# Performance work log

Measured on AMD Instinct MI355X. Metric: run time of the kernel, lower is better.

The kernel has to match this reference:

```python
import math
import jax, jax.numpy as jnp
import numpy as np

B, S, D, H = 2, 2048, 1024, 16


def setup_inputs() -> dict:
    key = jax.random.key(0)
    ks = jax.random.split(key, 8)
    scale = 1.0 / math.sqrt(D)
    kv_mask = jax.random.randint(ks[1], (B, S), 0, 2).astype(bool)
    kv_mask = kv_mask.at[:, 0].set(True)  # ensure at least one valid kv per batch
    return {
        "q": jax.random.normal(ks[0], (B, S, D), dtype=jnp.float32),
        "kv_mask": kv_mask,
        "Wq": jax.random.normal(ks[2], (D, D), dtype=jnp.float32) * scale,
        "Wk": jax.random.normal(ks[3], (D, D), dtype=jnp.float32) * scale,
        "Wv": jax.random.normal(ks[4], (D, D), dtype=jnp.float32) * scale,
        "Wo": jax.random.normal(ks[5], (D, D), dtype=jnp.float32) * scale,
        "bo": jax.random.normal(ks[6], (D,), dtype=jnp.float32) * 0.01,
        "num_heads": H,
    }


def _pass_with_mask(x, W, mask, b=None):
    # Linear applied everywhere, output zeroed where mask is False (pass_with_mask)
    y = x @ W.T
    if b is not None:
        y = y + b
    return jnp.where(mask[..., None], y, 0.0)


def reference(q, kv_mask, Wq, Wk, Wv, Wo, bo, num_heads):
    b, s, d = q.shape
    hd = d // num_heads
    q_mask = jnp.ones((b, s), dtype=bool)  # default q_mask in the module
    # self-attention: k = v = q
    qh = _pass_with_mask(q, Wq, q_mask).reshape(b, s, num_heads, hd)
    kh = _pass_with_mask(q, Wk, kv_mask).reshape(b, s, num_heads, hd)
    vh = _pass_with_mask(q, Wv, kv_mask).reshape(b, s, num_heads, hd)
    # scores: note the module scales by sqrt(model_dim), NOT sqrt(head_dim)
    scores = jnp.einsum("bqhd,bkhd->bhqk", qh, kh) / math.sqrt(d)
    mask = (q_mask[:, :, None] & kv_mask[:, None, :])[:, None, :, :]  # [b,1,q,k]
    scores = jnp.where(mask, scores, -jnp.inf)
    attn = jax.nn.softmax(scores, axis=-1)
    attn = jnp.where(mask, attn, 0.0)
    out = jnp.einsum("bhqk,bkhd->bqhd", attn, vh).reshape(b, s, d)
    return _pass_with_mask(out, Wo, q_mask, bo)
```

## Files before the change

kernel.cpp:

```cpp
#include <hip/hip_runtime.h>
#include <math.h>

#define B_ 2
#define S_ 2048
#define DM 1024
#define NH 16
#define HD 64

typedef unsigned short u16;
typedef unsigned int u32;
typedef __attribute__((ext_vector_type(8))) short bf16x8;
typedef __attribute__((ext_vector_type(4))) float f32x4;

#define C2SCALE 0.0450842200277800f

__device__ __forceinline__ u16 f2bf(float x) {
  unsigned u = __float_as_uint(x);
  u = (u + 0x7FFFu + ((u >> 16) & 1u)) >> 16;
  return (u16)u;
}

__device__ __forceinline__ u32 cvtpk(float lo, float hi) {
  u32 r;
  asm("v_cvt_pk_bf16_f32 %0, %1, %2" : "=v"(r) : "v"(lo), "v"(hi));
  return r;
}

__device__ __forceinline__ float exp2a(float x) {
  float r;
  asm("v_exp_f32 %0, %1" : "=v"(r) : "v"(x));
  return r;
}

__device__ __forceinline__ void gload_lds16(const u16* g, u16* l) {
  __builtin_amdgcn_global_load_lds((const __attribute__((address_space(1))) void*)g,
                                   (__attribute__((address_space(3))) void*)l, 16, 0, 0);
}

__device__ __forceinline__ int sigpos(int w6) {
  return ((w6 >> 5) << 5) | (((w6 >> 2) & 3) << 3) | (((w6 >> 4) & 1) << 2) | (w6 & 3);
}

__global__ void mask_scan(const int* __restrict__ kvm, int* __restrict__ posb,
                          int* __restrict__ nvb, u16* __restrict__ mwg) {
  const int b = blockIdx.x;
  const int tid = threadIdx.x;
  const int lane = tid & 63, wv = tid >> 6;
  __shared__ int wsum[4];
  int v[8], s = 0;
  const int base = b * S_ + tid * 8;
#pragma unroll
  for (int j = 0; j < 8; j++) { v[j] = kvm[base + j] ? 1 : 0; s += v[j]; }
  int sc = s;
#pragma unroll
  for (int off = 1; off < 64; off <<= 1) {
    int t = __shfl_up(sc, off, 64);
    if (lane >= off) sc += t;
  }
  if (lane == 63) wsum[wv] = sc;
  __syncthreads();
  int woff = 0;
#pragma unroll
  for (int w = 0; w < 4; w++) woff += (w < wv) ? wsum[w] : 0;
  int run = woff + sc - s;
#pragma unroll
  for (int j = 0; j < 8; j++) { posb[base + j] = run; run += v[j]; }
  const int total = wsum[0] + wsum[1] + wsum[2] + wsum[3];
  if (tid == 0) nvb[b] = total;
  for (int i = tid; i < S_; i += 256)
    mwg[b * S_ + (i & ~63) + sigpos(i & 63)] = (i < total) ? 0xFFFFu : 0u;
}

__global__ void cvt_all(const float* __restrict__ q, const float* __restrict__ Wq,
                        const float* __restrict__ Wk, const float* __restrict__ Wv,
                        const float* __restrict__ Wo, const int* __restrict__ nvb,
                        u16* __restrict__ Xbf, u16* __restrict__ Wcat,
                        u16* __restrict__ Wobf, u16* __restrict__ vtbuf) {
  const int NQ4 = (B_ * S_ * DM) / 4;
  const int NW4 = (DM * DM) / 4;
  const int total = NQ4 + 4 * NW4;
  int i = blockIdx.x * blockDim.x + threadIdx.x;
  int stride = gridDim.x * blockDim.x;
  for (int idx = i; idx < B_ * NH * HD * 64; idx += stride) {
    int col = idx & 63;
    int dd = (idx >> 6) & 63;
    int bh = idx >> 12;
    int nv = nvb[bh >> 4];
    int padw = ((nv + 63) & ~63) - nv;
    if (col < padw)
      vtbuf[((size_t)bh * HD + dd) * S_ + nv + col] = 0;
  }
  for (; i < total; i += stride) {
    const float* src;
    u16* dst;
    if (i < NQ4) {
      src = q + (size_t)i * 4; dst = Xbf + (size_t)i * 4;
    } else {
      int t = i - NQ4;
      if (t < NW4)            { src = Wq + (size_t)t * 4; dst = Wcat + (size_t)t * 4; }
      else if (t < 2 * NW4)   { src = Wk + (size_t)(t - NW4) * 4;     dst = Wcat + DM * DM + (size_t)(t - NW4) * 4; }
      else if (t < 3 * NW4)   { src = Wv + (size_t)(t - 2 * NW4) * 4; dst = Wcat + 2 * DM * DM + (size_t)(t - 2 * NW4) * 4; }
      else                    { src = Wo + (size_t)(t - 3 * NW4) * 4; dst = Wobf + (size_t)(t - 3 * NW4) * 4; }
    }
    float4 v = *(const float4*)src;
    ushort4 o;
    o.x = f2bf(v.x); o.y = f2bf(v.y); o.z = f2bf(v.z); o.w = f2bf(v.w);
    *(ushort4*)dst = o;
  }
}

__global__ __launch_bounds__(512, 6) void gemm_bt(
    const u16* __restrict__ A, const u16* __restrict__ Bw,
    u16* __restrict__ qo, u16* __restrict__ ko, u16* __restrict__ vo,
    const int* __restrict__ kvm, const int* __restrict__ posb) {
  __shared__ __align__(16) u16 As[2][64 * 64];
  __shared__ __align__(16) u16 Bs[2][64 * 64];
  const int K = DM;
  const int tid = threadIdx.x;
  const int wv = tid >> 6, lane = tid & 63;
  const int g = lane >> 4, c = lane & 15;
  const int wr = wv >> 1, wc = wv & 1;
  const int L = blockIdx.y * gridDim.x + blockIdx.x;
  const int cpx = (gridDim.x * gridDim.y) >> 3;
  const int Ls = (L & 7) * cpx + (L >> 3);
  const int Mb = (Ls & 31) << 7, Nb = (Ls >> 5) << 7;

  f32x4 acc[2][4];
#pragma unroll
  for (int i = 0; i < 2; i++)
#pragma unroll
    for (int j = 0; j < 4; j++) acc[i][j] = f32x4{0.f, 0.f, 0.f, 0.f};

  const int srow = tid >> 3;
  const int scol8 = tid & 7;
  const int m1 = srow * 2 + (scol8 >> 2);
  const int kkc = (scol8 & 3) * 8;
  const u16* ag = A + (size_t)(Mb + m1) * K + kkc;
  const u16* bg = Bw + (size_t)(Nb + m1) * K + kkc;
  const int slot = scol8 ^ (srow & 7);
  u16* al = &As[0][srow * 64 + slot * 8];
  u16* bl = &Bs[0][srow * 64 + slot * 8];

  bf16x8 ar = *(const bf16x8*)ag;
  bf16x8 br = *(const bf16x8*)bg;
  *(bf16x8*)al = ar;
  *(bf16x8*)bl = br;
  ar = *(const bf16x8*)(ag + 32);
  br = *(const bf16x8*)(bg + 32);
  __syncthreads();

  const int off = ((((c & 1) << 2) | g) ^ (c >> 1)) << 3;
  const int arb = (wr * 16 + (c >> 1)) * 64 + off;
  const int brb = (wc * 32 + (c >> 1)) * 64 + off;

  for (int t = 0; t < 32; ++t) {
    const int cur = t & 1;
    if (t + 1 < 32) {
      const int nb = (cur ^ 1) * 4096;
      *(bf16x8*)(al + nb) = ar;
      *(bf16x8*)(bl + nb) = br;
      if (t + 2 < 32) {
        ar = *(const bf16x8*)(ag + (t + 2) * 32);
        br = *(const bf16x8*)(bg + (t + 2) * 32);
      }
    }
    const u16* AB = &As[cur][0];
    const u16* BB = &Bs[cur][0];
    bf16x8 af[2], bfr[4];
#pragma unroll
    for (int mi = 0; mi < 2; mi++)
      af[mi] = *(const bf16x8*)&AB[arb + mi * 512];
#pragma unroll
    for (int ni = 0; ni < 4; ni++)
      bfr[ni] = *(const bf16x8*)&BB[brb + ni * 512];
#pragma unroll
    for (int mi = 0; mi < 2; mi++)
#pragma unroll
      for (int ni = 0; ni < 4; ni++)
        acc[mi][ni] = __builtin_amdgcn_mfma_f32_16x16x32_bf16(af[mi], bfr[ni], acc[mi][ni], 0, 0, 0);
    asm volatile("s_waitcnt lgkmcnt(0)\n\ts_barrier" ::: "memory");
  }

  const int nbase = Nb + wc * 64 + c;
  const int which = nbase >> 10;
  if (which == 0) {
#pragma unroll
    for (int mi = 0; mi < 2; mi++) {
#pragma unroll
      for (int ni = 0; ni < 4; ni++) {
        int nn = nbase + ni * 16;
        int h = nn >> 6, d = nn & 63;
#pragma unroll
        for (int r = 0; r < 4; r++) {
          int row = Mb + wr * 32 + mi * 16 + g * 4 + r;
          int b0 = row >> 11, s0 = row & 2047;
          qo[(((size_t)(b0 * NH + h)) * S_ + s0) * HD + d] =
              f2bf(acc[mi][ni][r] * C2SCALE);
        }
      }
    }
  } else if (which == 1) {
#pragma unroll
    for (int mi = 0; mi < 2; mi++) {
#pragma unroll
      for (int r = 0; r < 4; r++) {
        int row = Mb + wr * 32 + mi * 16 + g * 4 + r;
        int b0 = row >> 11, s0 = row & 2047;
        if (kvm[b0 * S_ + s0]) {
          int p = posb[b0 * S_ + s0];
#pragma unroll
          for (int ni = 0; ni < 4; ni++) {
            int nn = (nbase + ni * 16) & 1023;
            ko[((size_t)(b0 * NH + (nn >> 6)) * S_ + p) * HD + (nn & 63)] =
                f2bf(acc[mi][ni][r]);
          }
        }
      }
    }
  } else {
#pragma unroll
    for (int mi = 0; mi < 2; mi++) {
#pragma unroll
      for (int r = 0; r < 4; r++) {
        int row = Mb + wr * 32 + mi * 16 + g * 4 + r;
        int b0 = row >> 11, s0 = row & 2047;
        if (kvm[b0 * S_ + s0]) {
          int p = posb[b0 * S_ + s0];
          int dst = (p & ~63) + sigpos(p & 63);
#pragma unroll
          for (int ni = 0; ni < 4; ni++) {
            int nn = (nbase + ni * 16) & 1023;
            vo[((size_t)((b0 * NH + (nn >> 6)) * HD + (nn & 63))) * S_ + dst] =
                f2bf(acc[mi][ni][r]);
          }
        }
      }
    }
  }
}

__global__ __launch_bounds__(256, 4) void gemm_n64(
    const u16* __restrict__ A, const u16* __restrict__ Bw,
    const float* __restrict__ bias, float* __restrict__ fo) {
  __shared__ __align__(16) u16 As[128 * 32];
  __shared__ __align__(16) u16 Bs[64 * 32];
  const int K = DM, N = DM;
  const int tid = threadIdx.x;
  const int wv = tid >> 6, lane = tid & 63;
  const int g = lane >> 4, c = lane & 15;
  const int wr = wv >> 1, wc = wv & 1;
  const int L = blockIdx.x;
  const int Ls = (L & 7) * 64 + (L >> 3);
  const int Mb = (Ls & 31) << 7, Nb = (Ls >> 5) << 6;

  f32x4 acc[4][2];
#pragma unroll
  for (int i = 0; i < 4; i++)
#pragma unroll
    for (int j = 0; j < 2; j++) acc[i][j] = f32x4{0.f, 0.f, 0.f, 0.f};

  for (int kb = 0; kb < K; kb += 32) {
#pragma unroll
    for (int it = 0; it < 2; ++it) {
      int id = it * 256 + tid;
      int m = id >> 2, kk = (id & 3) * 8;
      gload_lds16(A + (size_t)(Mb + m) * K + kb + kk, As + (it * 4 + wv) * 512);
    }
    {
      int m = tid >> 2, kk = (tid & 3) * 8;
      gload_lds16(Bw + (size_t)(Nb + m) * K + kb + kk, Bs + wv * 512);
    }
    __syncthreads();
    bf16x8 af[4], bfr[2];
#pragma unroll
    for (int mi = 0; mi < 4; mi++)
      af[mi] = *(const bf16x8*)(As + (wr * 64 + mi * 16 + c) * 32 + g * 8);
#pragma unroll
    for (int ni = 0; ni < 2; ni++)
      bfr[ni] = *(const bf16x8*)(Bs + (wc * 32 + ni * 16 + c) * 32 + g * 8);
#pragma unroll
    for (int mi = 0; mi < 4; mi++)
#pragma unroll
      for (int ni = 0; ni < 2; ni++)
        acc[mi][ni] = __builtin_amdgcn_mfma_f32_16x16x32_bf16(af[mi], bfr[ni], acc[mi][ni], 0, 0, 0);
    __syncthreads();
  }

#pragma unroll
  for (int mi = 0; mi < 4; mi++) {
#pragma unroll
    for (int ni = 0; ni < 2; ni++) {
      int n = Nb + wc * 32 + ni * 16 + c;
      float bv = bias[n];
#pragma unroll
      for (int r = 0; r < 4; r++) {
        int row = Mb + wr * 64 + mi * 16 + g * 4 + r;
        fo[(size_t)row * N + n] = acc[mi][ni][r] + bv;
      }
    }
  }
}

__global__ __launch_bounds__(512, 4) void attn_kernel(
    const u16* __restrict__ qb, const u16* __restrict__ kb,
    const u16* __restrict__ vtb, const u16* __restrict__ mwg,
    const int* __restrict__ nvb, u16* __restrict__ ob) {
  __shared__ __align__(16) u16 Kl[2][64 * 64];
  __shared__ __align__(16) u16 Vl[2][64 * 64];
  __shared__ __align__(16) u16 MW[S_];

  const int tid = threadIdx.x;
  const int wv = tid >> 6, lane = tid & 63;
  const int g = lane >> 4, c = lane & 15;

  const int L = blockIdx.x;
  const int j = L >> 3;
  const int bh = ((L & 7) << 2) | (j >> 4);
  const int qi = j & 15;
  const int b = bh >> 4, h = bh & 15;
  const int q0 = qi * 128;
  const size_t bhbase = (size_t)bh * (S_ * HD);
  const int NT = (nvb[b] + 63) >> 6;

  ((uint2*)MW)[tid] = ((const uint2*)(mwg + b * S_))[tid];

  bf16x8 qf[2];
#pragma unroll
  for (int ks = 0; ks < 2; ks++)
    qf[ks] = *(const bf16x8*)(qb + bhbase + (size_t)(q0 + wv * 16 + c) * HD + ks * 32 + g * 8);

  f32x4 Oa[4];
#pragma unroll
  for (int di = 0; di < 4; di++) Oa[di] = f32x4{0.f, 0.f, 0.f, 0.f};
  f32x4 lacc = f32x4{0.f, 0.f, 0.f, 0.f};

  union { u32 u[4]; bf16x8 v; } ones;
#pragma unroll
  for (int w = 0; w < 4; w++) ones.u[w] = 0x3F803F80u;

  const int srow = tid >> 3;
  const int scol8 = tid & 7;
  const u16* kg = kb + bhbase + (size_t)srow * HD + scol8 * 8;
  const u16* vg = vtb + bhbase + (size_t)srow * S_ + scol8 * 8;
  const int wslot = scol8 ^ (srow & 7);
  u16* kld = &Kl[0][srow * 64 + wslot * 8];
  u16* vld = &Vl[0][srow * 64 + wslot * 8];

  bf16x8 krg = *(const bf16x8*)kg;
  bf16x8 vrg = *(const bf16x8*)vg;
  *(bf16x8*)kld = krg;
  *(bf16x8*)vld = vrg;
  krg = *(const bf16x8*)(kg + 64 * HD);
  vrg = *(const bf16x8*)(vg + 64);
  __syncthreads();

  const int swz = c & 7;

  for (int t = 0; t < NT; ++t) {
    const int cur = t & 1;
    if (t + 1 < NT) {
      *(bf16x8*)(kld + (cur ^ 1) * 4096) = krg;
      *(bf16x8*)(vld + (cur ^ 1) * 4096) = vrg;
      if (t + 2 < NT) {
        krg = *(const bf16x8*)(kg + (t + 2) * (64 * HD));
        vrg = *(const bf16x8*)(vg + (t + 2) * 64);
      }
    }
    const u16* KB = &Kl[cur][0];
    const u16* VB = &Vl[cur][0];

    f32x4 Sa[4];
#pragma unroll
    for (int ni = 0; ni < 4; ni++) Sa[ni] = f32x4{0.f, 0.f, 0.f, 0.f};
    __builtin_amdgcn_s_setprio(1);
#pragma unroll
    for (int ks = 0; ks < 2; ks++) {
      bf16x8 kf[4];
#pragma unroll
      for (int ni = 0; ni < 4; ni++)
        kf[ni] = *(const bf16x8*)&KB[(ni * 16 + c) * 64 + (((4 * ks + g) ^ swz) * 8)];
#pragma unroll
      for (int ni = 0; ni < 4; ni++)
        Sa[ni] = __builtin_amdgcn_mfma_f32_16x16x32_bf16(kf[ni], qf[ks], Sa[ni], 0, 0, 0);
    }
    __builtin_amdgcn_s_setprio(0);

    bf16x8 Pa[2];
#pragma unroll
    for (int ks = 0; ks < 2; ks++) {
      uint4 mw = *(const uint4*)&MW[t * 64 + ks * 32 + g * 8];
      union { u32 u[4]; bf16x8 v; } pw;
      pw.u[0] = cvtpk(exp2a(Sa[2 * ks][0]), exp2a(Sa[2 * ks][1])) & mw.x;
      pw.u[1] = cvtpk(exp2a(Sa[2 * ks][2]), exp2a(Sa[2 * ks][3])) & mw.y;
      pw.u[2] = cvtpk(exp2a(Sa[2 * ks + 1][0]), exp2a(Sa[2 * ks + 1][1])) & mw.z;
      pw.u[3] = cvtpk(exp2a(Sa[2 * ks + 1][2]), exp2a(Sa[2 * ks + 1][3])) & mw.w;
      Pa[ks] = pw.v;
    }

    __builtin_amdgcn_s_setprio(1);
    lacc = __builtin_amdgcn_mfma_f32_16x16x32_bf16(ones.v, Pa[0], lacc, 0, 0, 0);
    lacc = __builtin_amdgcn_mfma_f32_16x16x32_bf16(ones.v, Pa[1], lacc, 0, 0, 0);
#pragma unroll
    for (int ks = 0; ks < 2; ks++) {
      bf16x8 vf[4];
#pragma unroll
      for (int di = 0; di < 4; di++)
        vf[di] = *(const bf16x8*)&VB[(di * 16 + c) * 64 + (((4 * ks + g) ^ swz) * 8)];
#pragma unroll
      for (int di = 0; di < 4; di++)
        Oa[di] = __builtin_amdgcn_mfma_f32_16x16x32_bf16(vf[di], Pa[ks], Oa[di], 0, 0, 0);
    }
    __builtin_amdgcn_s_setprio(0);

    asm volatile("s_waitcnt lgkmcnt(0)\n\ts_barrier" ::: "memory");
  }

  float inv = 1.f / lacc[0];
  int q = q0 + wv * 16 + c;
  size_t base = ((size_t)(b * S_ + q)) * DM + (size_t)h * HD;
#pragma unroll
  for (int di = 0; di < 4; di++) {
    uint2 o;
    o.x = cvtpk(Oa[di][0] * inv, Oa[di][1] * inv);
    o.y = cvtpk(Oa[di][2] * inv, Oa[di][3] * inv);
    *(uint2*)(ob + base + di * 16 + g * 4) = o;
  }
}

extern "C" void kernel_launch(void* const* d_in, const int* in_sizes, int n_in,
                              void* d_out, int out_size, void* d_ws, size_t ws_size,
                              hipStream_t stream) {
  const float* q  = (const float*)d_in[0];
  const int* kvm  = (const int*)d_in[1];
  const float* Wq = (const float*)d_in[2];
  const float* Wk = (const float*)d_in[3];
  const float* Wv = (const float*)d_in[4];
  const float* Wo = (const float*)d_in[5];
  const float* bo = (const float*)d_in[6];
  float* out = (float*)d_out;
  char* ws = (char*)d_ws;

  u16* Xbf   = (u16*)(ws);
  u16* Wcat  = (u16*)(ws + (8u << 20));
  u16* Wobf  = (u16*)(ws + (14u << 20));
  u16* qbuf  = (u16*)(ws + (16u << 20));
  u16* kbuf  = (u16*)(ws + (24u << 20));
  u16* vtbuf = (u16*)(ws + (32u << 20));
  u16* mwg   = (u16*)(ws + (40u << 20));
  int* posb  = (int*)(ws + (41u << 20));
  int* nvb   = (int*)(ws + (42u << 20));
  u16* obuf  = Xbf;

  mask_scan<<<B_, 256, 0, stream>>>(kvm, posb, nvb, mwg);
  cvt_all<<<2048, 256, 0, stream>>>(q, Wq, Wk, Wv, Wo, nvb, Xbf, Wcat, Wobf, vtbuf);
  gemm_bt<<<dim3(32, 24), 512, 0, stream>>>(Xbf, Wcat, qbuf, kbuf, vtbuf,
                                            kvm, posb);
  attn_kernel<<<512, 512, 0, stream>>>(qbuf, kbuf, vtbuf, mwg, nvb, obuf);
  gemm_n64<<<512, 256, 0, stream>>>(obuf, Wobf, bo, out);
}
```

Baseline: 109.3 us.

## Compact valid KV rows before K/V projection and skip masked-row GEMM tiles

The conversion kernel now also scatters valid (kv_mask true) rows of the bf16 input into a compacted buffer, which reuses the output allocation as scratch. The QKV GEMM is restructured into a 1D grid: Q tiles use the full input, while K/V tiles read the compacted rows and exit early for tiles beyond the valid count. Because roughly half the keys are masked, this cuts about half the K/V projection FLOPs and replaces per-row mask/position lookups in the epilogue with a simple bound check. In exchange it adds an extra scattered write of the input and relies on the output buffer being free until the final GEMM.

```diff
diff --git a/kernel.cpp b/kernel.cpp
--- a/kernel.cpp
+++ b/kernel.cpp
@@ -73,9 +73,11 @@
 
 __global__ void cvt_all(const float* __restrict__ q, const float* __restrict__ Wq,
                         const float* __restrict__ Wk, const float* __restrict__ Wv,
-                        const float* __restrict__ Wo, const int* __restrict__ nvb,
+                        const float* __restrict__ Wo, const int* __restrict__ kvm,
+                        const int* __restrict__ posb, const int* __restrict__ nvb,
                         u16* __restrict__ Xbf, u16* __restrict__ Wcat,
-                        u16* __restrict__ Wobf, u16* __restrict__ vtbuf) {
+                        u16* __restrict__ Wobf, u16* __restrict__ vtbuf,
+                        u16* __restrict__ Xc) {
   const int NQ4 = (B_ * S_ * DM) / 4;
   const int NW4 = (DM * DM) / 4;
   const int total = NQ4 + 4 * NW4;
@@ -91,39 +93,64 @@
       vtbuf[((size_t)bh * HD + dd) * S_ + nv + col] = 0;
   }
   for (; i < total; i += stride) {
-    const float* src;
-    u16* dst;
     if (i < NQ4) {
-      src = q + (size_t)i * 4; dst = Xbf + (size_t)i * 4;
+      float4 v = ((const float4*)q)[i];
+      ushort4 o;
+      o.x = f2bf(v.x); o.y = f2bf(v.y); o.z = f2bf(v.z); o.w = f2bf(v.w);
+      ((ushort4*)Xbf)[i] = o;
+      int row = i >> 8, chunk = i & 255;
+      int b = row >> 11, s = row & 2047;
+      if (kvm[b * S_ + s]) {
+        int p = posb[b * S_ + s];
+        *(ushort4*)(Xc + ((size_t)(b * S_ + p)) * DM + chunk * 4) = o;
+      }
     } else {
       int t = i - NQ4;
+      const float* src;
+      u16* dst;
       if (t < NW4)            { src = Wq + (size_t)t * 4; dst = Wcat + (size_t)t * 4; }
       else if (t < 2 * NW4)   { src = Wk + (size_t)(t - NW4) * 4;     dst = Wcat + DM * DM + (size_t)(t - NW4) * 4; }
       else if (t < 3 * NW4)   { src = Wv + (size_t)(t - 2 * NW4) * 4; dst = Wcat + 2 * DM * DM + (size_t)(t - 2 * NW4) * 4; }
       else                    { src = Wo + (size_t)(t - 3 * NW4) * 4; dst = Wobf + (size_t)(t - 3 * NW4) * 4; }
-    }
-    float4 v = *(const float4*)src;
-    ushort4 o;
-    o.x = f2bf(v.x); o.y = f2bf(v.y); o.z = f2bf(v.z); o.w = f2bf(v.w);
-    *(ushort4*)dst = o;
-  }
-}
-
-__global__ __launch_bounds__(512, 6) void gemm_bt(
-    const u16* __restrict__ A, const u16* __restrict__ Bw,
-    u16* __restrict__ qo, u16* __restrict__ ko, u16* __restrict__ vo,
-    const int* __restrict__ kvm, const int* __restrict__ posb) {
+      float4 v = *(const float4*)src;
+      ushort4 o;
+      o.x = f2bf(v.x); o.y = f2bf(v.y); o.z = f2bf(v.z); o.w = f2bf(v.w);
+      *(ushort4*)dst = o;
+    }
+  }
+}
+
+__global__ __launch_bounds__(512, 6) void gemm_qkv(
+    const u16* __restrict__ Xbf, const u16* __restrict__ Xc,
+    const u16* __restrict__ Wcat, u16* __restrict__ qo, u16* __restrict__ ko,
+    u16* __restrict__ vo, const int* __restrict__ nvb) {
+  const int K = DM;
+  const int Lraw = blockIdx.x;
+  const int Ls = (Lraw & 7) * 96 + (Lraw >> 3);
+
+  int Mb, nglob, bkv = 0, nv = 1 << 30;
+  const u16* Ap;
+  if (Ls < 256) {
+    Mb = (Ls & 31) << 7;
+    nglob = (Ls >> 5) << 7;
+    Ap = Xbf;
+  } else {
+    int L2 = Ls - 256;
+    bkv = L2 >> 8;
+    int L3 = L2 & 255;
+    Mb = (L3 & 15) << 7;
+    nglob = 1024 + ((L3 >> 4) << 7);
+    nv = nvb[bkv];
+    if (Mb >= nv) return;
+    Ap = Xc + (size_t)bkv * S_ * DM;
+  }
+
   __shared__ __align__(16) u16 As[2][64 * 64];
   __shared__ __align__(16) u16 Bs[2][64 * 64];
-  const int K = DM;
   const int tid = threadIdx.x;
   const int wv = tid >> 6, lane = tid & 63;
   const int g = lane >> 4, c = lane & 15;
   const int wr = wv >> 1, wc = wv & 1;
-  const int L = blockIdx.y * gridDim.x + blockIdx.x;
-  const int cpx = (gridDim.x * gridDim.y) >> 3;
-  const int Ls = (L & 7) * cpx + (L >> 3);
-  const int Mb = (Ls & 31) << 7, Nb = (Ls >> 5) << 7;
 
   f32x4 acc[2][4];
 #pragma unroll
@@ -135,8 +162,8 @@
   const int scol8 = tid & 7;
   const int m1 = srow * 2 + (scol8 >> 2);
   const int kkc = (scol8 & 3) * 8;
-  const u16* ag = A + (size_t)(Mb + m1) * K + kkc;
-  const u16* bg = Bw + (size_t)(Nb + m1) * K + kkc;
+  const u16* ag = Ap + (size_t)(Mb + m1) * K + kkc;
+  const u16* bg = Wcat + (size_t)(nglob + m1) * K + kkc;
   const int slot = scol8 ^ (srow & 7);
   u16* al = &As[0][srow * 64 + slot * 8];
   u16* bl = &Bs[0][srow * 64 + slot * 8];
@@ -181,7 +208,7 @@
     asm volatile("s_waitcnt lgkmcnt(0)\n\ts_barrier" ::: "memory");
   }
 
-  const int nbase = Nb + wc * 64 + c;
+  const int nbase = nglob + wc * 64 + c;
   const int which = nbase >> 10;
   if (which == 0) {
 #pragma unroll
@@ -204,14 +231,12 @@
     for (int mi = 0; mi < 2; mi++) {
 #pragma unroll
       for (int r = 0; r < 4; r++) {
-        int row = Mb + wr * 32 + mi * 16 + g * 4 + r;
-        int b0 = row >> 11, s0 = row & 2047;
-        if (kvm[b0 * S_ + s0]) {
-          int p = posb[b0 * S_ + s0];
+        int p = Mb + wr * 32 + mi * 16 + g * 4 + r;
+        if (p < nv) {
 #pragma unroll
           for (int ni = 0; ni < 4; ni++) {
             int nn = (nbase + ni * 16) & 1023;
-            ko[((size_t)(b0 * NH + (nn >> 6)) * S_ + p) * HD + (nn & 63)] =
+            ko[((size_t)(bkv * NH + (nn >> 6)) * S_ + p) * HD + (nn & 63)] =
                 f2bf(acc[mi][ni][r]);
           }
         }
@@ -222,15 +247,13 @@
     for (int mi = 0; mi < 2; mi++) {
 #pragma unroll
       for (int r = 0; r < 4; r++) {
-        int row = Mb + wr * 32 + mi * 16 + g * 4 + r;
-        int b0 = row >> 11, s0 = row & 2047;
-        if (kvm[b0 * S_ + s0]) {
-          int p = posb[b0 * S_ + s0];
+        int p = Mb + wr * 32 + mi * 16 + g * 4 + r;
+        if (p < nv) {
           int dst = (p & ~63) + sigpos(p & 63);
 #pragma unroll
           for (int ni = 0; ni < 4; ni++) {
             int nn = (nbase + ni * 16) & 1023;
-            vo[((size_t)((b0 * NH + (nn >> 6)) * HD + (nn & 63))) * S_ + dst] =
+            vo[((size_t)((bkv * NH + (nn >> 6)) * HD + (nn & 63))) * S_ + dst] =
                 f2bf(acc[mi][ni][r]);
           }
         }
@@ -449,12 +472,13 @@
   u16* mwg   = (u16*)(ws + (40u << 20));
   int* posb  = (int*)(ws + (41u << 20));
   int* nvb   = (int*)(ws + (42u << 20));
+  u16* Xc    = (u16*)d_out;
   u16* obuf  = Xbf;
 
   mask_scan<<<B_, 256, 0, stream>>>(kvm, posb, nvb, mwg);
-  cvt_all<<<2048, 256, 0, stream>>>(q, Wq, Wk, Wv, Wo, nvb, Xbf, Wcat, Wobf, vtbuf);
-  gemm_bt<<<dim3(32, 24), 512, 0, stream>>>(Xbf, Wcat, qbuf, kbuf, vtbuf,
-                                            kvm, posb);
+  cvt_all<<<2048, 256, 0, stream>>>(q, Wq, Wk, Wv, Wo, kvm, posb, nvb,
+                                    Xbf, Wcat, Wobf, vtbuf, Xc);
+  gemm_qkv<<<768, 512, 0, stream>>>(Xbf, Xc, Wcat, qbuf, kbuf, vtbuf, nvb);
   attn_kernel<<<512, 512, 0, stream>>>(qbuf, kbuf, vtbuf, mwg, nvb, obuf);
   gemm_n64<<<512, 256, 0, stream>>>(obuf, Wobf, bo, out);
 }
```

Result: no change. 110.3 us (+0.9%).
